# Kernel tuning notes

Hardware: AMD Instinct MI355X
Metric: run time of the kernel (lower is better)

The kernel has to match this reference:

```python
import jax, jax.numpy as jnp
import numpy as np

K = 31  # AvgPool2d kernel size
P = 15  # padding


def _box_avg(x):
    """31x31 stride-1 avg pool, count_include_pad=True (PyTorch default):
    separable ones-conv with zero padding, divided by K*K."""
    B, C, H, W = x.shape
    kh = jnp.ones((C, 1, K, 1), x.dtype)
    kw = jnp.ones((C, 1, 1, K), x.dtype)
    dn = ('NCHW', 'OIHW', 'NCHW')
    y = jax.lax.conv_general_dilated(x, kh, (1, 1), [(P, P), (0, 0)],
                                     dimension_numbers=dn, feature_group_count=C)
    y = jax.lax.conv_general_dilated(y, kw, (1, 1), [(0, 0), (P, P)],
                                     dimension_numbers=dn, feature_group_count=C)
    return y / (K * K)


def setup_inputs() -> dict:
    key = jax.random.key(0)
    k1, k2 = jax.random.split(key)
    pred = jax.random.normal(k1, (64, 1, 512, 512), dtype=jnp.float32)
    mask = jax.random.uniform(k2, (64, 1, 512, 512), dtype=jnp.float32)
    return {"pred": pred, "mask": mask}


def reference(pred, mask):
    weit = 1.0 + 5.0 * jnp.abs(_box_avg(mask) - mask)
    p = jax.nn.sigmoid(pred)
    inter = jnp.sum(p * mask * weit, axis=(2, 3))          # [B, C]
    union = jnp.sum((p + mask) * weit, axis=(2, 3))        # [B, C]
    wdiss = 1.0 - (2.0 * inter + 0.5) / (union + 0.5)
    return jnp.mean(wdiss)
```

## Files before the change

kernel.cpp:

```cpp
#include <hip/hip_runtime.h>
#include <math.h>

#define NB 64
#define HH 512
#define WW 512
#define KK 31
#define PP 15
#define TSP 128
#define NSP (HH / TSP)
#define RING 64
#define RMASK (RING - 1)

typedef _Float16 f16;
typedef f16 f16x8 __attribute__((ext_vector_type(8)));
typedef f16 f16x4 __attribute__((ext_vector_type(4)));
typedef f16 f16x2 __attribute__((ext_vector_type(2)));

__device__ __forceinline__ f16x2 shfl_up2(f16x2 v, int delta) {
    int x = __shfl_up(__builtin_bit_cast(int, v), delta);
    return __builtin_bit_cast(f16x2, x);
}
__device__ __forceinline__ f16x2 shfl_dn2(f16x2 v, int delta) {
    int x = __shfl_down(__builtin_bit_cast(int, v), delta);
    return __builtin_bit_cast(f16x2, x);
}
__device__ __forceinline__ f16x2 sel2(bool c, f16x2 v) {
    f16x2 z = {(f16)0, (f16)0};
    return c ? v : z;
}

template<int NK, bool CHECK>
__device__ __forceinline__ void phase1_pairs(
        const float* __restrict__ mb, f16 (* __restrict__ Hs)[WW],
        f16 (* __restrict__ Ms)[WW],
        const int y0, const int pfirst, const int wave, const int lane)
{
    const int xbase = lane * 8;
    const bool lm1 = (lane >= 1);
    const bool lm2 = (lane >= 2);
    const bool lp1 = (lane <= 62);
    const bool lp2 = (lane <= 61);

    #pragma unroll
    for (int k = 0; k < NK; ++k) {
        const int p = pfirst + k * 8 + wave;
        if (CHECK && p > 30) continue;
        const int h0  = 2 * p;
        const int gy0 = y0 + h0 - PP;
        const int gy1 = gy0 + 1;

        float va[8], vb[8];
        if (gy0 >= 0 && gy0 < HH) {
            const float* row = mb + (size_t)gy0 * WW + xbase;
            const float4 u = *(const float4*)(row);
            const float4 v = *(const float4*)(row + 4);
            va[0] = u.x; va[1] = u.y; va[2] = u.z; va[3] = u.w;
            va[4] = v.x; va[5] = v.y; va[6] = v.z; va[7] = v.w;
        } else {
            #pragma unroll
            for (int j = 0; j < 8; ++j) va[j] = 0.0f;
        }
        if (gy1 >= 0 && gy1 < HH) {
            const float* row = mb + (size_t)gy1 * WW + xbase;
            const float4 u = *(const float4*)(row);
            const float4 v = *(const float4*)(row + 4);
            vb[0] = u.x; vb[1] = u.y; vb[2] = u.z; vb[3] = u.w;
            vb[4] = v.x; vb[5] = v.y; vb[6] = v.z; vb[7] = v.w;
        } else {
            #pragma unroll
            for (int j = 0; j < 8; ++j) vb[j] = 0.0f;
        }

        const int yr0 = h0 - PP;
        if (yr0 >= 0 && yr0 < TSP) {
            f16x8 mv;
            #pragma unroll
            for (int j = 0; j < 8; ++j) mv[j] = (f16)va[j];
            *(f16x8*)&Ms[yr0 & RMASK][xbase] = mv;
        }
        if (yr0 + 1 >= 0 && yr0 + 1 < TSP) {
            f16x8 mv;
            #pragma unroll
            for (int j = 0; j < 8; ++j) mv[j] = (f16)vb[j];
            *(f16x8*)&Ms[(yr0 + 1) & RMASK][xbase] = mv;
        }

        float sa[8], sb[8];
        sa[0] = va[0]; sb[0] = vb[0];
        #pragma unroll
        for (int j = 1; j < 8; ++j) { sa[j] = sa[j-1] + va[j]; sb[j] = sb[j-1] + vb[j]; }

        f16x2 ps[8];
        #pragma unroll
        for (int j = 0; j < 8; ++j)
            ps[j] = __builtin_bit_cast(f16x2, __builtin_amdgcn_cvt_pkrtz(sa[j], sb[j]));
        const f16x2 pT = ps[7];

        f16x2 A[7];
        #pragma unroll
        for (int j = 0; j < 7; ++j) A[j] = shfl_up2(pT - ps[j], 2);
        const f16x2 Bprev = shfl_up2(pT, 1);
        const f16x2 Cfull = shfl_dn2(pT, 1);
        f16x2 Cp[7];
        #pragma unroll
        for (int j = 0; j < 7; ++j) Cp[j] = shfl_dn2(ps[j], 2);

        f16x2 base = pT;
        base += sel2(lm1, Bprev);
        base += sel2(lp1, Cfull);

        f16x8 ha, hb;
        #pragma unroll
        for (int j = 0; j < 8; ++j) {
            f16x2 acc = base;
            if (j < 7) acc += sel2(lm2, A[j]);
            if (j > 0) acc += sel2(lp2, Cp[j-1]);
            ha[j] = acc[0];
            hb[j] = acc[1];
        }
        *(f16x8*)&Hs[h0 & RMASK][xbase] = ha;
        *(f16x8*)&Hs[(h0 + 1) & RMASK][xbase] = hb;
    }
}

__device__ __forceinline__ void phase2_half(
        const float* __restrict__ pb,
        const f16 (* __restrict__ Hs)[WW], const f16 (* __restrict__ Ms)[WW],
        const int y0, const int r0h, const int c,
        float4& I4, float4& U4)
{
    f16x4 hl8[8], he8[8];
    f16x4 accA = {(f16)0, (f16)0, (f16)0, (f16)0};
    f16x4 accB = {(f16)0, (f16)0, (f16)0, (f16)0};
    #pragma unroll
    for (int j = 0; j < 8; ++j) {
        hl8[j] = *(const f16x4*)&Hs[(r0h + j) & RMASK][c];
        accA += hl8[j];
    }
    #pragma unroll
    for (int j = 8; j < 15; ++j) accA += *(const f16x4*)&Hs[(r0h + j) & RMASK][c];
    #pragma unroll
    for (int j = 15; j < 30; ++j) accB += *(const f16x4*)&Hs[(r0h + j) & RMASK][c];
    #pragma unroll
    for (int i = 0; i < 8; ++i) he8[i] = *(const f16x4*)&Hs[(r0h + 30 + i) & RMASK][c];

    float4 B;
    B.x = (float)accA[0] + (float)accB[0];
    B.y = (float)accA[1] + (float)accB[1];
    B.z = (float)accA[2] + (float)accB[2];
    B.w = (float)accA[3] + (float)accB[3];

    const float inv2 = 1.0f / (float)(KK * KK);

    #pragma unroll
    for (int i = 0; i < 8; ++i) {
        const int yr = r0h + i;
        const f16x4 he = he8[i];
        const f16x4 hl = hl8[i];
        const f16x4 mm = *(const f16x4*)&Ms[yr & RMASK][c];
        const float4 p4 = *(const float4*)(pb + (size_t)(y0 + yr) * WW + c);
        const float m0 = (float)mm[0], m1 = (float)mm[1];
        const float m2 = (float)mm[2], m3 = (float)mm[3];

        B.x += (float)he[0]; B.y += (float)he[1]; B.z += (float)he[2]; B.w += (float)he[3];

        const float w0 = fmaf(5.0f, fabsf(fmaf(B.x, inv2, -m0)), 1.0f);
        const float w1 = fmaf(5.0f, fabsf(fmaf(B.y, inv2, -m1)), 1.0f);
        const float w2 = fmaf(5.0f, fabsf(fmaf(B.z, inv2, -m2)), 1.0f);
        const float w3 = fmaf(5.0f, fabsf(fmaf(B.w, inv2, -m3)), 1.0f);
        const float sg0 = __builtin_amdgcn_rcpf(1.0f + __expf(-p4.x));
        const float sg1 = __builtin_amdgcn_rcpf(1.0f + __expf(-p4.y));
        const float sg2 = __builtin_amdgcn_rcpf(1.0f + __expf(-p4.z));
        const float sg3 = __builtin_amdgcn_rcpf(1.0f + __expf(-p4.w));

        I4.x = fmaf(sg0 * m0, w0, I4.x);  U4.x = fmaf(sg0 + m0, w0, U4.x);
        I4.y = fmaf(sg1 * m1, w1, I4.y);  U4.y = fmaf(sg1 + m1, w1, U4.y);
        I4.z = fmaf(sg2 * m2, w2, I4.z);  U4.z = fmaf(sg2 + m2, w2, U4.z);
        I4.w = fmaf(sg3 * m3, w3, I4.w);  U4.w = fmaf(sg3 + m3, w3, U4.w);

        B.x -= (float)hl[0]; B.y -= (float)hl[1]; B.z -= (float)hl[2]; B.w -= (float)hl[3];
    }
}


__global__ __launch_bounds__(512, 2) void dice_fused_kernel(
        const float* __restrict__ pred,
        const float* __restrict__ mask,
        float* __restrict__ part) {
    const int sp = blockIdx.x;
    const int b  = blockIdx.y;
    const int t  = threadIdx.x;
    const int wave = t >> 6;
    const int lane = t & 63;

    __shared__ f16 Hs[RING][WW];
    __shared__ f16 Ms[RING][WW];
    __shared__ float red[16];

    const float* mb = mask + (size_t)b * HH * WW;
    const float* pb = pred + (size_t)b * HH * WW;
    const int y0 = sp * TSP;

    phase1_pairs<4, true>(mb, Hs, Ms, y0, 0, wave, lane);
    __syncthreads();

    const int q = t & 127;
    const int g = t >> 7;
    const int c = q * 4;

    float4 I4 = make_float4(0.f, 0.f, 0.f, 0.f);
    float4 U4 = make_float4(0.f, 0.f, 0.f, 0.f);

    #pragma unroll
    for (int half = 0; half < 4; ++half) {
        phase2_half(pb, Hs, Ms, y0, g * 8 + 32 * half, c, I4, U4);
        __syncthreads();
        if (half < 3) {
            phase1_pairs<2, false>(mb, Hs, Ms, y0, 31 + 16 * half, wave, lane);
            __syncthreads();
        }
    }

    float inter = I4.x + I4.y + I4.z + I4.w;
    float uni   = U4.x + U4.y + U4.z + U4.w;
    #pragma unroll
    for (int off = 32; off > 0; off >>= 1) {
        inter += __shfl_down(inter, off);
        uni   += __shfl_down(uni, off);
    }
    if (lane == 0) { red[wave] = inter; red[8 + wave] = uni; }
    __syncthreads();
    if (t == 0) {
        float ti = 0.f, tu = 0.f;
        #pragma unroll
        for (int w2 = 0; w2 < 8; ++w2) { ti += red[w2]; tu += red[8 + w2]; }
        const int bid = b * NSP + sp;
        part[bid] = ti;
        part[NB * NSP + bid] = tu;
    }
}

__global__ void dice_final_kernel(const float* __restrict__ part,
                                  float* __restrict__ out) {
    const int t = threadIdx.x;
    float inter = 0.0f, uni = 0.0f;
    #pragma unroll
    for (int s = 0; s < NSP; ++s) {
        inter += part[t * NSP + s];
        uni   += part[NB * NSP + t * NSP + s];
    }
    float wd = 1.0f - (2.0f * inter + 0.5f) / (uni + 0.5f);
    #pragma unroll
    for (int off = 32; off > 0; off >>= 1) wd += __shfl_down(wd, off);
    if (t == 0) out[0] = wd * (1.0f / (float)NB);
}

extern "C" void kernel_launch(void* const* d_in, const int* in_sizes, int n_in,
                              void* d_out, int out_size, void* d_ws, size_t ws_size,
                              hipStream_t stream) {
    const float* pred = (const float*)d_in[0];
    const float* mask = (const float*)d_in[1];
    float* out  = (float*)d_out;
    float* part = (float*)d_ws;

    dim3 grid(NSP, NB);
    dice_fused_kernel<<<grid, 512, 0, stream>>>(pred, mask, part);
    dice_final_kernel<<<1, 64, 0, stream>>>(part, out);
}
```

Before: 146.4 us.

## Double block size to 1024 threads and prefetch pred rows in phase 2

Raises the block from 512 to 1024 threads (16 waves) and redistributes the work: each wave now handles half as many row pairs in the horizontal box-sum phase, and each thread handles 4 output rows per phase-2 pass instead of 8. Pred values are loaded up front into registers before the LDS reads for the vertical sum, which hides global load latency. The aim is more latency hiding per block on the same 128 KB LDS footprint. In exchange, each thread recomputes the 30-row vertical window sum for half as many outputs, which adds redundant LDS reads. The launch bound of 4 blocks of 1024 threads per CU is also unlikely to be reachable given the LDS use.

```diff
diff --git a/kernel.cpp b/kernel.cpp
--- a/kernel.cpp
+++ b/kernel.cpp
@@ -10,6 +10,8 @@
 #define NSP (HH / TSP)
 #define RING 64
 #define RMASK (RING - 1)
+#define NT 1024
+#define NWAVE (NT / 64)
 
 typedef _Float16 f16;
 typedef f16 f16x8 __attribute__((ext_vector_type(8)));
@@ -43,7 +45,7 @@
 
     #pragma unroll
     for (int k = 0; k < NK; ++k) {
-        const int p = pfirst + k * 8 + wave;
+        const int p = pfirst + k * 16 + wave;
         if (CHECK && p > 30) continue;
         const int h0  = 2 * p;
         const int gy0 = y0 + h0 - PP;
@@ -129,20 +131,25 @@
         const int y0, const int r0h, const int c,
         float4& I4, float4& U4)
 {
-    f16x4 hl8[8], he8[8];
+    float4 Pq[4];
+    #pragma unroll
+    for (int i = 0; i < 4; ++i)
+        Pq[i] = *(const float4*)(pb + (size_t)(y0 + r0h + i) * WW + c);
+
+    f16x4 hl4[4], he4[4];
     f16x4 accA = {(f16)0, (f16)0, (f16)0, (f16)0};
     f16x4 accB = {(f16)0, (f16)0, (f16)0, (f16)0};
     #pragma unroll
-    for (int j = 0; j < 8; ++j) {
-        hl8[j] = *(const f16x4*)&Hs[(r0h + j) & RMASK][c];
-        accA += hl8[j];
-    }
-    #pragma unroll
-    for (int j = 8; j < 15; ++j) accA += *(const f16x4*)&Hs[(r0h + j) & RMASK][c];
+    for (int j = 0; j < 4; ++j) {
+        hl4[j] = *(const f16x4*)&Hs[(r0h + j) & RMASK][c];
+        accA += hl4[j];
+    }
+    #pragma unroll
+    for (int j = 4; j < 15; ++j) accA += *(const f16x4*)&Hs[(r0h + j) & RMASK][c];
     #pragma unroll
     for (int j = 15; j < 30; ++j) accB += *(const f16x4*)&Hs[(r0h + j) & RMASK][c];
     #pragma unroll
-    for (int i = 0; i < 8; ++i) he8[i] = *(const f16x4*)&Hs[(r0h + 30 + i) & RMASK][c];
+    for (int i = 0; i < 4; ++i) he4[i] = *(const f16x4*)&Hs[(r0h + 30 + i) & RMASK][c];
 
     float4 B;
     B.x = (float)accA[0] + (float)accB[0];
@@ -153,12 +160,12 @@
     const float inv2 = 1.0f / (float)(KK * KK);
 
     #pragma unroll
-    for (int i = 0; i < 8; ++i) {
+    for (int i = 0; i < 4; ++i) {
         const int yr = r0h + i;
-        const f16x4 he = he8[i];
-        const f16x4 hl = hl8[i];
+        const f16x4 he = he4[i];
+        const f16x4 hl = hl4[i];
         const f16x4 mm = *(const f16x4*)&Ms[yr & RMASK][c];
-        const float4 p4 = *(const float4*)(pb + (size_t)(y0 + yr) * WW + c);
+        const float4 p4 = Pq[i];
         const float m0 = (float)mm[0], m1 = (float)mm[1];
         const float m2 = (float)mm[2], m3 = (float)mm[3];
 
@@ -183,7 +190,7 @@
 }
 
 
-__global__ __launch_bounds__(512, 2) void dice_fused_kernel(
+__global__ __launch_bounds__(NT, 4) void dice_fused_kernel(
         const float* __restrict__ pred,
         const float* __restrict__ mask,
         float* __restrict__ part) {
@@ -195,13 +202,13 @@
 
     __shared__ f16 Hs[RING][WW];
     __shared__ f16 Ms[RING][WW];
-    __shared__ float red[16];
+    __shared__ float red[2 * NWAVE];
 
     const float* mb = mask + (size_t)b * HH * WW;
     const float* pb = pred + (size_t)b * HH * WW;
     const int y0 = sp * TSP;
 
-    phase1_pairs<4, true>(mb, Hs, Ms, y0, 0, wave, lane);
+    phase1_pairs<2, true>(mb, Hs, Ms, y0, 0, wave, lane);
     __syncthreads();
 
     const int q = t & 127;
@@ -213,10 +220,10 @@
 
     #pragma unroll
     for (int half = 0; half < 4; ++half) {
-        phase2_half(pb, Hs, Ms, y0, g * 8 + 32 * half, c, I4, U4);
+        phase2_half(pb, Hs, Ms, y0, 32 * half + g * 4, c, I4, U4);
         __syncthreads();
         if (half < 3) {
-            phase1_pairs<2, false>(mb, Hs, Ms, y0, 31 + 16 * half, wave, lane);
+            phase1_pairs<1, false>(mb, Hs, Ms, y0, 31 + 16 * half, wave, lane);
             __syncthreads();
         }
     }
@@ -228,12 +235,12 @@
         inter += __shfl_down(inter, off);
         uni   += __shfl_down(uni, off);
     }
-    if (lane == 0) { red[wave] = inter; red[8 + wave] = uni; }
+    if (lane == 0) { red[wave] = inter; red[NWAVE + wave] = uni; }
     __syncthreads();
     if (t == 0) {
         float ti = 0.f, tu = 0.f;
         #pragma unroll
-        for (int w2 = 0; w2 < 8; ++w2) { ti += red[w2]; tu += red[8 + w2]; }
+        for (int w2 = 0; w2 < NWAVE; ++w2) { ti += red[w2]; tu += red[NWAVE + w2]; }
         const int bid = b * NSP + sp;
         part[bid] = ti;
         part[NB * NSP + bid] = tu;
@@ -264,6 +271,6 @@
     float* part = (float*)d_ws;
 
     dim3 grid(NSP, NB);
-    dice_fused_kernel<<<grid, 512, 0, stream>>>(pred, mask, part);
+    dice_fused_kernel<<<grid, NT, 0, stream>>>(pred, mask, part);
     dice_final_kernel<<<1, 64, 0, stream>>>(part, out);
 }
```

After: 157.4 us. 7.6% more time.

## Prefetch next mask rows and pred rows ahead of phase-2 compute

Applied to the files above, without the earlier changes.

Splits the horizontal-sum stage into a load step and a compute step. The global mask loads for the next ring slice are issued before the current phase-2 pass, so their latency overlaps the vertical-sum and loss work. Phase 2 also loads all eight pred rows up front behind a compiler scheduling barrier rather than one per iteration. This raises register pressure (32 extra floats for mask plus 32 for pred), which can hurt occupancy at the 512x2 launch bound.

```diff
diff --git a/kernel.cpp b/kernel.cpp
--- a/kernel.cpp
+++ b/kernel.cpp
@@ -28,99 +28,96 @@
     f16x2 z = {(f16)0, (f16)0};
     return c ? v : z;
 }
-
-template<int NK, bool CHECK>
-__device__ __forceinline__ void phase1_pairs(
-        const float* __restrict__ mb, f16 (* __restrict__ Hs)[WW],
-        f16 (* __restrict__ Ms)[WW],
-        const int y0, const int pfirst, const int wave, const int lane)
+__device__ __forceinline__ void memfence_sched() { asm volatile("" ::: "memory"); }
+
+__device__ __forceinline__ void load_pair(
+        const float* __restrict__ mb, const int y0, const int p,
+        const int xbase, float (&va)[8], float (&vb)[8])
 {
-    const int xbase = lane * 8;
+    const int gy0 = y0 + 2 * p - PP;
+    const int gy1 = gy0 + 1;
+    if (gy0 >= 0 && gy0 < HH) {
+        const float* row = mb + (size_t)gy0 * WW + xbase;
+        const float4 u = *(const float4*)(row);
+        const float4 v = *(const float4*)(row + 4);
+        va[0] = u.x; va[1] = u.y; va[2] = u.z; va[3] = u.w;
+        va[4] = v.x; va[5] = v.y; va[6] = v.z; va[7] = v.w;
+    } else {
+        #pragma unroll
+        for (int j = 0; j < 8; ++j) va[j] = 0.0f;
+    }
+    if (gy1 >= 0 && gy1 < HH) {
+        const float* row = mb + (size_t)gy1 * WW + xbase;
+        const float4 u = *(const float4*)(row);
+        const float4 v = *(const float4*)(row + 4);
+        vb[0] = u.x; vb[1] = u.y; vb[2] = u.z; vb[3] = u.w;
+        vb[4] = v.x; vb[5] = v.y; vb[6] = v.z; vb[7] = v.w;
+    } else {
+        #pragma unroll
+        for (int j = 0; j < 8; ++j) vb[j] = 0.0f;
+    }
+}
+
+__device__ __forceinline__ void compute_pair(
+        f16 (* __restrict__ Hs)[WW], f16 (* __restrict__ Ms)[WW],
+        const int p, const int xbase, const int lane,
+        const float (&va)[8], const float (&vb)[8])
+{
     const bool lm1 = (lane >= 1);
     const bool lm2 = (lane >= 2);
     const bool lp1 = (lane <= 62);
     const bool lp2 = (lane <= 61);
-
-    #pragma unroll
-    for (int k = 0; k < NK; ++k) {
-        const int p = pfirst + k * 8 + wave;
-        if (CHECK && p > 30) continue;
-        const int h0  = 2 * p;
-        const int gy0 = y0 + h0 - PP;
-        const int gy1 = gy0 + 1;
-
-        float va[8], vb[8];
-        if (gy0 >= 0 && gy0 < HH) {
-            const float* row = mb + (size_t)gy0 * WW + xbase;
-            const float4 u = *(const float4*)(row);
-            const float4 v = *(const float4*)(row + 4);
-            va[0] = u.x; va[1] = u.y; va[2] = u.z; va[3] = u.w;
-            va[4] = v.x; va[5] = v.y; va[6] = v.z; va[7] = v.w;
-        } else {
-            #pragma unroll
-            for (int j = 0; j < 8; ++j) va[j] = 0.0f;
-        }
-        if (gy1 >= 0 && gy1 < HH) {
-            const float* row = mb + (size_t)gy1 * WW + xbase;
-            const float4 u = *(const float4*)(row);
-            const float4 v = *(const float4*)(row + 4);
-            vb[0] = u.x; vb[1] = u.y; vb[2] = u.z; vb[3] = u.w;
-            vb[4] = v.x; vb[5] = v.y; vb[6] = v.z; vb[7] = v.w;
-        } else {
-            #pragma unroll
-            for (int j = 0; j < 8; ++j) vb[j] = 0.0f;
-        }
-
-        const int yr0 = h0 - PP;
-        if (yr0 >= 0 && yr0 < TSP) {
-            f16x8 mv;
-            #pragma unroll
-            for (int j = 0; j < 8; ++j) mv[j] = (f16)va[j];
-            *(f16x8*)&Ms[yr0 & RMASK][xbase] = mv;
-        }
-        if (yr0 + 1 >= 0 && yr0 + 1 < TSP) {
-            f16x8 mv;
-            #pragma unroll
-            for (int j = 0; j < 8; ++j) mv[j] = (f16)vb[j];
-            *(f16x8*)&Ms[(yr0 + 1) & RMASK][xbase] = mv;
-        }
-
-        float sa[8], sb[8];
-        sa[0] = va[0]; sb[0] = vb[0];
-        #pragma unroll
-        for (int j = 1; j < 8; ++j) { sa[j] = sa[j-1] + va[j]; sb[j] = sb[j-1] + vb[j]; }
-
-        f16x2 ps[8];
-        #pragma unroll
-        for (int j = 0; j < 8; ++j)
-            ps[j] = __builtin_bit_cast(f16x2, __builtin_amdgcn_cvt_pkrtz(sa[j], sb[j]));
-        const f16x2 pT = ps[7];
-
-        f16x2 A[7];
-        #pragma unroll
-        for (int j = 0; j < 7; ++j) A[j] = shfl_up2(pT - ps[j], 2);
-        const f16x2 Bprev = shfl_up2(pT, 1);
-        const f16x2 Cfull = shfl_dn2(pT, 1);
-        f16x2 Cp[7];
-        #pragma unroll
-        for (int j = 0; j < 7; ++j) Cp[j] = shfl_dn2(ps[j], 2);
-
-        f16x2 base = pT;
-        base += sel2(lm1, Bprev);
-        base += sel2(lp1, Cfull);
-
-        f16x8 ha, hb;
-        #pragma unroll
-        for (int j = 0; j < 8; ++j) {
-            f16x2 acc = base;
-            if (j < 7) acc += sel2(lm2, A[j]);
-            if (j > 0) acc += sel2(lp2, Cp[j-1]);
-            ha[j] = acc[0];
-            hb[j] = acc[1];
-        }
-        *(f16x8*)&Hs[h0 & RMASK][xbase] = ha;
-        *(f16x8*)&Hs[(h0 + 1) & RMASK][xbase] = hb;
-    }
+    const int h0 = 2 * p;
+
+    const int yr0 = h0 - PP;
+    if (yr0 >= 0 && yr0 < TSP) {
+        f16x8 mv;
+        #pragma unroll
+        for (int j = 0; j < 8; ++j) mv[j] = (f16)va[j];
+        *(f16x8*)&Ms[yr0 & RMASK][xbase] = mv;
+    }
+    if (yr0 + 1 >= 0 && yr0 + 1 < TSP) {
+        f16x8 mv;
+        #pragma unroll
+        for (int j = 0; j < 8; ++j) mv[j] = (f16)vb[j];
+        *(f16x8*)&Ms[(yr0 + 1) & RMASK][xbase] = mv;
+    }
+
+    float sa[8], sb[8];
+    sa[0] = va[0]; sb[0] = vb[0];
+    #pragma unroll
+    for (int j = 1; j < 8; ++j) { sa[j] = sa[j-1] + va[j]; sb[j] = sb[j-1] + vb[j]; }
+
+    f16x2 ps[8];
+    #pragma unroll
+    for (int j = 0; j < 8; ++j)
+        ps[j] = __builtin_bit_cast(f16x2, __builtin_amdgcn_cvt_pkrtz(sa[j], sb[j]));
+    const f16x2 pT = ps[7];
+
+    f16x2 A[7];
+    #pragma unroll
+    for (int j = 0; j < 7; ++j) A[j] = shfl_up2(pT - ps[j], 2);
+    const f16x2 Bprev = shfl_up2(pT, 1);
+    const f16x2 Cfull = shfl_dn2(pT, 1);
+    f16x2 Cp[7];
+    #pragma unroll
+    for (int j = 0; j < 7; ++j) Cp[j] = shfl_dn2(ps[j], 2);
+
+    f16x2 base = pT;
+    base += sel2(lm1, Bprev);
+    base += sel2(lp1, Cfull);
+
+    f16x8 ha, hb;
+    #pragma unroll
+    for (int j = 0; j < 8; ++j) {
+        f16x2 acc = base;
+        if (j < 7) acc += sel2(lm2, A[j]);
+        if (j > 0) acc += sel2(lp2, Cp[j-1]);
+        ha[j] = acc[0];
+        hb[j] = acc[1];
+    }
+    *(f16x8*)&Hs[h0 & RMASK][xbase] = ha;
+    *(f16x8*)&Hs[(h0 + 1) & RMASK][xbase] = hb;
 }
 
 __device__ __forceinline__ void phase2_half(
@@ -129,6 +126,12 @@
         const int y0, const int r0h, const int c,
         float4& I4, float4& U4)
 {
+    float4 Pq[8];
+    #pragma unroll
+    for (int i = 0; i < 8; ++i)
+        Pq[i] = *(const float4*)(pb + (size_t)(y0 + r0h + i) * WW + c);
+    memfence_sched();
+
     f16x4 hl8[8], he8[8];
     f16x4 accA = {(f16)0, (f16)0, (f16)0, (f16)0};
     f16x4 accB = {(f16)0, (f16)0, (f16)0, (f16)0};
@@ -158,7 +161,7 @@
         const f16x4 he = he8[i];
         const f16x4 hl = hl8[i];
         const f16x4 mm = *(const f16x4*)&Ms[yr & RMASK][c];
-        const float4 p4 = *(const float4*)(pb + (size_t)(y0 + yr) * WW + c);
+        const float4 p4 = Pq[i];
         const float m0 = (float)mm[0], m1 = (float)mm[1];
         const float m2 = (float)mm[2], m3 = (float)mm[3];
 
@@ -192,6 +195,7 @@
     const int t  = threadIdx.x;
     const int wave = t >> 6;
     const int lane = t & 63;
+    const int xbase = lane * 8;
 
     __shared__ f16 Hs[RING][WW];
     __shared__ f16 Ms[RING][WW];
@@ -201,7 +205,14 @@
     const float* pb = pred + (size_t)b * HH * WW;
     const int y0 = sp * TSP;
 
-    phase1_pairs<4, true>(mb, Hs, Ms, y0, 0, wave, lane);
+    #pragma unroll
+    for (int k = 0; k < 4; ++k) {
+        const int p = k * 8 + wave;
+        if (p > 30) continue;
+        float va[8], vb[8];
+        load_pair(mb, y0, p, xbase, va, vb);
+        compute_pair(Hs, Ms, p, xbase, lane, va, vb);
+    }
     __syncthreads();
 
     const int q = t & 127;
@@ -211,12 +222,21 @@
     float4 I4 = make_float4(0.f, 0.f, 0.f, 0.f);
     float4 U4 = make_float4(0.f, 0.f, 0.f, 0.f);
 
+    float va0[8], vb0[8], va1[8], vb1[8];
+
     #pragma unroll
     for (int half = 0; half < 4; ++half) {
-        phase2_half(pb, Hs, Ms, y0, g * 8 + 32 * half, c, I4, U4);
+        const int pf = 31 + 16 * half + wave;
+        if (half < 3) {
+            load_pair(mb, y0, pf,     xbase, va0, vb0);
+            load_pair(mb, y0, pf + 8, xbase, va1, vb1);
+            memfence_sched();
+        }
+        phase2_half(pb, Hs, Ms, y0, 32 * half + g * 8, c, I4, U4);
         __syncthreads();
         if (half < 3) {
-            phase1_pairs<2, false>(mb, Hs, Ms, y0, 31 + 16 * half, wave, lane);
+            compute_pair(Hs, Ms, pf,     xbase, lane, va0, vb0);
+            compute_pair(Hs, Ms, pf + 8, xbase, lane, va1, vb1);
             __syncthreads();
         }
     }
```

Measured after the change: 146.6 us. Within noise of the previous version (+0.2%).
